# Kernel optimization log

Measured on AMD Instinct MI355X. Metric: run time of the kernel, lower is better.

Reference implementation:

```python
import jax, jax.numpy as jnp
import numpy as np

EPS_NORM = 1e-9   # l2_norm eps in original
EPS_ENT = 1e-15   # PyG dense_diff_pool entropy eps


def _sage_block(x, adj, Wl, bl, Wr):
    """SAGEConv(aggr='mean') + ReLU + row L2-norm.
    x: [b,N,din], adj: [b,N,N] binary (adj[i,j]=1 means edge i->j).
    PyG mean-aggr for target j = mean over sources i: (A^T x)/max(deg_in,1).
    out = lin_l(aggr) + lin_r(x); lin_l has bias, lin_r does not.
    """
    deg = jnp.sum(adj, axis=1)                                  # [b,N] in-degree of targets
    agg = jnp.einsum('bij,bid->bjd', adj, x) / jnp.maximum(deg, 1.0)[..., None]
    h = jnp.einsum('bnd,od->bno', agg, Wl) + bl + jnp.einsum('bnd,od->bno', x, Wr)
    h = jax.nn.relu(h)
    return h / (jnp.linalg.norm(h, axis=-1, keepdims=True) + EPS_NORM)


def setup_inputs() -> dict:
    key = jax.random.key(0)
    ks = jax.random.split(key, 16)
    b, N, din, dh, K = 8, 2048, 128, 128, 128
    x = jax.random.normal(ks[0], (b, N, din), dtype=jnp.float32)
    # binary adjacency, avg in-degree ~ 0.01*N ~ 20
    adj = (jax.random.uniform(ks[1], (b, N, N)) < 0.01).astype(jnp.float32)

    def lin(k, o, i):
        return (jax.random.normal(k, (o, i), dtype=jnp.float32) / np.sqrt(i)).astype(jnp.float32)

    return {
        'x': x, 'adj': adj,
        'We1l': lin(ks[2], dh, din), 'be1': jnp.zeros((dh,), jnp.float32), 'We1r': lin(ks[3], dh, din),
        'We2l': lin(ks[4], dh, dh),  'be2': jnp.zeros((dh,), jnp.float32), 'We2r': lin(ks[5], dh, dh),
        'Wa1l': lin(ks[6], dh, din), 'ba1': jnp.zeros((dh,), jnp.float32), 'Wa1r': lin(ks[7], dh, din),
        'Wa2l': lin(ks[8], K, dh),   'ba2': jnp.zeros((K,), jnp.float32), 'Wa2r': lin(ks[9], K, dh),
    }


def reference(x, adj, We1l, be1, We1r, We2l, be2, We2r, Wa1l, ba1, Wa1r, Wa2l, ba2, Wa2r):
    # embedding GNN
    h = _sage_block(x, adj, We1l, be1, We1r)
    h_emb = _sage_block(h, adj, We2l, be2, We2r)          # [b,N,dh]
    # assignment GNN
    a = _sage_block(x, adj, Wa1l, ba1, Wa1r)
    a = _sage_block(a, adj, Wa2l, ba2, Wa2r)              # [b,N,K]
    S = jax.nn.softmax(a, axis=-1)                        # [b,N,K]
    # dense_diff_pool
    h_pooled = jnp.einsum('bnk,bnd->bkd', S, h_emb)       # [b,K,dh]
    adj_pooled = jnp.einsum('bnk,bnm,bml->bkl', S, adj, S)  # [b,K,K]
    link = adj - jnp.einsum('bnk,bmk->bnm', S, S)
    link_loss = jnp.linalg.norm(link) / adj.size          # global Frobenius / numel
    ent_loss = jnp.mean(jnp.sum(-S * jnp.log(S + EPS_ENT), axis=-1))
    return h_pooled, adj_pooled, link_loss, ent_loss
```

## Files before the change

### kernel.cpp

```cpp
#include <hip/hip_runtime.h>
#include <hip/hip_bf16.h>
#include <math.h>

#define BB 8
#define NN 2048
#define DD 128
#define SPL 16
#define CAPQ 32

typedef __bf16 bf16x8 __attribute__((ext_vector_type(8)));
typedef float f32x4 __attribute__((ext_vector_type(4)));

__device__ inline unsigned short f2bu(float f) {
  __hip_bfloat16 h = __float2bfloat16(f);
  return *reinterpret_cast<unsigned short*>(&h);
}
__device__ inline unsigned int pack2(float a, float b) {
  return (unsigned int)f2bu(a) | ((unsigned int)f2bu(b) << 16);
}
__device__ inline float blo(unsigned u) { return __uint_as_float(u << 16); }
__device__ inline float bhi(unsigned u) { return __uint_as_float(u & 0xffff0000u); }

__global__ __launch_bounds__(256) void k_build(const float* __restrict__ adj,
                                               unsigned short* __restrict__ colidx,
                                               float* __restrict__ deg,
                                               float* __restrict__ rdeg,
                                               double* __restrict__ scal) {
  __shared__ float T[2][64][65];
  __shared__ unsigned short L[64][4][CAPQ];
  __shared__ int cnts[64][4];
  __shared__ float tsum[64];
  int b = blockIdx.y, j0 = blockIdx.x * 64;
  const float* A = adj + (size_t)b * NN * NN + j0;
  int t = threadIdx.x;
  int lr = t >> 2, lc0 = (t & 3) * 16;
  int sc = t & 63, sq = t >> 6;
  float4 pre[4];
  #pragma unroll
  for (int e = 0; e < 4; ++e)
    pre[e] = *(const float4*)(A + (size_t)lr * NN + lc0 + e * 4);
  #pragma unroll
  for (int e = 0; e < 4; ++e)
    *(float4*)&T[0][lr][lc0 + e * 4] = pre[e];
  __syncthreads();
  int cnt = 0;
  for (int ch = 0; ch < 32; ++ch) {
    if (ch + 1 < 32) {
      const float* src = A + (size_t)(ch + 1) * 64 * NN;
      #pragma unroll
      for (int e = 0; e < 4; ++e)
        pre[e] = *(const float4*)(src + (size_t)lr * NN + lc0 + e * 4);
    }
    #pragma unroll
    for (int p = 0; p < 16; ++p) {
      int il = sq * 16 + p;
      float v = T[ch & 1][il][sc];
      if (v != 0.f) {
        L[sc][sq][cnt < CAPQ ? cnt : CAPQ - 1] = (unsigned short)(ch * 64 + il);
        ++cnt;
      }
    }
    if (ch + 1 < 32) {
      #pragma unroll
      for (int e = 0; e < 4; ++e)
        *(float4*)&T[(ch + 1) & 1][lr][lc0 + e * 4] = pre[e];
    }
    __syncthreads();
  }
  cnts[sc][sq] = cnt;
  __syncthreads();
  int c = t >> 2, seg = t & 3;
  int n0 = cnts[c][0], n1 = cnts[c][1], n2 = cnts[c][2], n3 = cnts[c][3];
  int tot = n0 + n1 + n2 + n3;
  unsigned short vals[16];
  #pragma unroll
  for (int e = 0; e < 16; ++e) {
    int k = seg * 16 + e;
    unsigned short x = 0;
    if (k < n0) x = L[c][0][k];
    else if (k < n0 + n1) x = L[c][1][k - n0];
    else if (k < n0 + n1 + n2) x = L[c][2][k - n0 - n1];
    else if (k < tot) x = L[c][3][k - n0 - n1 - n2];
    vals[e] = x;
  }
  unsigned short* dst = colidx + ((size_t)b * NN + j0 + c) * 64 + seg * 16;
  *(uint4*)dst = *(uint4*)&vals[0];
  *(uint4*)(dst + 8) = *(uint4*)&vals[8];
  if (seg == 0) {
    size_t gj = (size_t)b * NN + j0 + c;
    deg[gj] = (float)tot;
    rdeg[gj] = 1.f / fmaxf((float)tot, 1.f);
    tsum[c] = (float)tot;
  }
  __syncthreads();
  if (t < 64) {
    float s = tsum[t];
    #pragma unroll
    for (int off = 32; off > 0; off >>= 1) s += __shfl_xor(s, off);
    if (t == 0) atomicAdd(scal, (double)s);
  }
}

__global__ __launch_bounds__(256) void k_xbf(const float* __restrict__ x,
                                             __hip_bfloat16* __restrict__ xb) {
  size_t i8 = ((size_t)blockIdx.x * 256 + threadIdx.x) * 8;
  float4 a = *(const float4*)(x + i8);
  float4 b2 = *(const float4*)(x + i8 + 4);
  unsigned r[4] = {pack2(a.x, a.y), pack2(a.z, a.w), pack2(b2.x, b2.y), pack2(b2.z, b2.w)};
  *(uint4*)((unsigned short*)xb + i8) = *(uint4*)r;
}

__global__ __launch_bounds__(256) void k_agg(const __hip_bfloat16* __restrict__ V,
                                             const unsigned short* __restrict__ colidx,
                                             const float* __restrict__ deg,
                                             const float* __restrict__ rdeg,
                                             __hip_bfloat16* __restrict__ out) {
  int w = threadIdx.x >> 6, l = threadIdx.x & 63;
  size_t jg = (size_t)blockIdx.x * 4 + w;
  int b = (int)(jg >> 11);
  int cnt = (int)deg[jg];
  int myi = colidx[jg * 64 + l];
  const unsigned short* Vb = (const unsigned short*)V + (((size_t)b << 11)) * DD;
  float ax = 0.f, ay = 0.f;
  int k = 0;
  for (; k + 4 <= cnt; k += 4) {
    int i0 = __shfl(myi, k), i1 = __shfl(myi, k + 1);
    int i2 = __shfl(myi, k + 2), i3 = __shfl(myi, k + 3);
    unsigned u0 = *(const unsigned*)(Vb + (size_t)i0 * DD + 2 * l);
    unsigned u1 = *(const unsigned*)(Vb + (size_t)i1 * DD + 2 * l);
    unsigned u2 = *(const unsigned*)(Vb + (size_t)i2 * DD + 2 * l);
    unsigned u3 = *(const unsigned*)(Vb + (size_t)i3 * DD + 2 * l);
    ax += blo(u0) + blo(u1) + blo(u2) + blo(u3);
    ay += bhi(u0) + bhi(u1) + bhi(u2) + bhi(u3);
  }
  for (; k < cnt; ++k) {
    int i0 = __shfl(myi, k);
    unsigned u0 = *(const unsigned*)(Vb + (size_t)i0 * DD + 2 * l);
    ax += blo(u0); ay += bhi(u0);
  }
  float sc = rdeg[jg];
  *(unsigned*)((unsigned short*)out + jg * DD + 2 * l) = pack2(ax * sc, ay * sc);
}

__global__ __launch_bounds__(256) void k_agg2(const __hip_bfloat16* __restrict__ V1,
                                              const __hip_bfloat16* __restrict__ V2,
                                              const unsigned short* __restrict__ colidx,
                                              const float* __restrict__ deg,
                                              const float* __restrict__ rdeg,
                                              __hip_bfloat16* __restrict__ out1,
                                              __hip_bfloat16* __restrict__ out2) {
  int w = threadIdx.x >> 6, l = threadIdx.x & 63;
  size_t jg = (size_t)blockIdx.x * 4 + w;
  int b = (int)(jg >> 11);
  int cnt = (int)deg[jg];
  int myi = colidx[jg * 64 + l];
  size_t base = (((size_t)b << 11)) * DD + 2 * l;
  const unsigned short* Va = (const unsigned short*)V1 + base;
  const unsigned short* Vb = (const unsigned short*)V2 + base;
  float ax = 0.f, ay = 0.f, bx = 0.f, by = 0.f;
  int k = 0;
  for (; k + 2 <= cnt; k += 2) {
    int i0 = __shfl(myi, k), i1 = __shfl(myi, k + 1);
    unsigned a0 = *(const unsigned*)(Va + (size_t)i0 * DD);
    unsigned a1 = *(const unsigned*)(Va + (size_t)i1 * DD);
    unsigned b0 = *(const unsigned*)(Vb + (size_t)i0 * DD);
    unsigned b1 = *(const unsigned*)(Vb + (size_t)i1 * DD);
    ax += blo(a0) + blo(a1); ay += bhi(a0) + bhi(a1);
    bx += blo(b0) + blo(b1); by += bhi(b0) + bhi(b1);
  }
  if (k < cnt) {
    int i0 = __shfl(myi, k);
    unsigned a0 = *(const unsigned*)(Va + (size_t)i0 * DD);
    unsigned b0 = *(const unsigned*)(Vb + (size_t)i0 * DD);
    ax += blo(a0); ay += bhi(a0);
    bx += blo(b0); by += bhi(b0);
  }
  float sc = rdeg[jg];
  *(unsigned*)((unsigned short*)out1 + jg * DD + 2 * l) = pack2(ax * sc, ay * sc);
  *(unsigned*)((unsigned short*)out2 + jg * DD + 2 * l) = pack2(bx * sc, by * sc);
}

__global__ __launch_bounds__(256) void k_aggT(const __hip_bfloat16* __restrict__ Sbf,
                                              const unsigned short* __restrict__ colidx,
                                              const float* __restrict__ deg,
                                              __hip_bfloat16* __restrict__ PT) {
  __shared__ float Lt[128][17];
  int w = threadIdx.x >> 6, l = threadIdx.x & 63;
  size_t jbase = (size_t)blockIdx.x * 16;
  int b = (int)(jbase >> 11);
  const unsigned short* Vb = (const unsigned short*)Sbf + (((size_t)b << 11)) * DD;
  #pragma unroll
  for (int cc = 0; cc < 4; ++cc) {
    int jl = w * 4 + cc;
    size_t jg = jbase + jl;
    int cnt = (int)deg[jg];
    int myi = colidx[jg * 64 + l];
    float ax = 0.f, ay = 0.f;
    int k = 0;
    for (; k + 4 <= cnt; k += 4) {
      int i0 = __shfl(myi, k), i1 = __shfl(myi, k + 1);
      int i2 = __shfl(myi, k + 2), i3 = __shfl(myi, k + 3);
      unsigned u0 = *(const unsigned*)(Vb + (size_t)i0 * DD + 2 * l);
      unsigned u1 = *(const unsigned*)(Vb + (size_t)i1 * DD + 2 * l);
      unsigned u2 = *(const unsigned*)(Vb + (size_t)i2 * DD + 2 * l);
      unsigned u3 = *(const unsigned*)(Vb + (size_t)i3 * DD + 2 * l);
      ax += blo(u0) + blo(u1) + blo(u2) + blo(u3);
      ay += bhi(u0) + bhi(u1) + bhi(u2) + bhi(u3);
    }
    for (; k < cnt; ++k) {
      int i0 = __shfl(myi, k);
      unsigned u0 = *(const unsigned*)(Vb + (size_t)i0 * DD + 2 * l);
      ax += blo(u0); ay += bhi(u0);
    }
    Lt[2 * l][jl] = ax;
    Lt[2 * l + 1][jl] = ay;
  }
  __syncthreads();
  int t = threadIdx.x;
  if (t < 128) {
    int j0 = (int)(jbase & (NN - 1));
    unsigned wv[8];
    #pragma unroll
    for (int e = 0; e < 8; ++e)
      wv[e] = pack2(Lt[t][2 * e], Lt[t][2 * e + 1]);
    unsigned short* dst = (unsigned short*)PT + ((size_t)b * DD + t) * NN + j0;
    *(uint4*)dst = *(uint4*)&wv[0];
    *(uint4*)(dst + 8) = *(uint4*)&wv[4];
  }
}

__global__ __launch_bounds__(256) void k_linred(const __hip_bfloat16* __restrict__ AGG,
                                                const __hip_bfloat16* __restrict__ X2,
                                                const float* __restrict__ W1,
                                                const float* __restrict__ W2,
                                                const float* __restrict__ bias,
                                                float* __restrict__ outf,
                                                __hip_bfloat16* __restrict__ outbf,
                                                __hip_bfloat16* __restrict__ outT) {
  __shared__ __align__(16) char smem[64 * 136 * 2 * 2];
  __shared__ __align__(16) __hip_bfloat16 Wsm[128 * 72];
  __shared__ float bsm[128];
  __hip_bfloat16* As = (__hip_bfloat16*)smem;
  __hip_bfloat16* Xs = As + 64 * 136;
  float* Ho = (float*)smem;

  int b = blockIdx.y, j0 = blockIdx.x * 64;
  int t = threadIdx.x;
  size_t rowbase = (size_t)b * NN + j0;

  if (t < 128) bsm[t] = bias[t];
  #pragma unroll
  for (int e = 0; e < 8; ++e) {
    int idx = t + e * 256;
    int r = idx >> 5, c4 = idx & 31;
    size_t g = (rowbase + r) * DD + c4 * 4;
    *(uint2*)&As[r * 136 + c4 * 4] = *(const uint2*)((const unsigned short*)AGG + g);
    *(uint2*)&Xs[r * 136 + c4 * 4] = *(const uint2*)((const unsigned short*)X2 + g);
  }
  __syncthreads();

  int w = t >> 6, l = t & 63;
  int lm = l & 15, lq = l >> 4;
  int jloc = w * 16 + lm;
  f32x4 acc[8];
  #pragma unroll
  for (int mt = 0; mt < 8; ++mt)
    #pragma unroll
    for (int r = 0; r < 4; ++r) acc[mt][r] = 0.f;

  #pragma unroll
  for (int ph = 0; ph < 2; ++ph) {
    const __hip_bfloat16* Xt = ph ? Xs : As;
    const float* W = ph ? W2 : W1;
    #pragma unroll
    for (int ch = 0; ch < 2; ++ch) {
      __syncthreads();
      #pragma unroll
      for (int e = 0; e < 8; ++e) {
        int idx = t + e * 256;
        int o = idx >> 4, k4 = idx & 15;
        float4 wv = *(const float4*)(W + o * DD + ch * 64 + k4 * 4);
        uint2 pw; pw.x = pack2(wv.x, wv.y); pw.y = pack2(wv.z, wv.w);
        *(uint2*)&Wsm[o * 72 + k4 * 4] = pw;
      }
      __syncthreads();
      #pragma unroll
      for (int s = 0; s < 2; ++s) {
        int kx = ch * 64 + s * 32 + lq * 8;
        bf16x8 bfr = *(const bf16x8*)&Xt[jloc * 136 + kx];
        int kw = s * 32 + lq * 8;
        #pragma unroll
        for (int mt = 0; mt < 8; ++mt) {
          bf16x8 afr = *(const bf16x8*)&Wsm[(mt * 16 + lm) * 72 + kw];
          acc[mt] = __builtin_amdgcn_mfma_f32_16x16x32_bf16(afr, bfr, acc[mt], 0, 0, 0);
        }
      }
    }
  }

  __syncthreads();
  float hv[8][4];
  float psum = 0.f;
  #pragma unroll
  for (int mt = 0; mt < 8; ++mt)
    #pragma unroll
    for (int r = 0; r < 4; ++r) {
      int o = mt * 16 + lq * 4 + r;
      float v = fmaxf(acc[mt][r] + bsm[o], 0.f);
      hv[mt][r] = v;
      psum += v * v;
    }
  psum += __shfl_xor(psum, 16);
  psum += __shfl_xor(psum, 32);
  float rn = 1.f / (sqrtf(psum) + 1e-9f);
  #pragma unroll
  for (int mt = 0; mt < 8; ++mt)
    #pragma unroll
    for (int r = 0; r < 4; ++r) {
      int o = mt * 16 + lq * 4 + r;
      Ho[jloc * 132 + o] = hv[mt][r] * rn;
    }
  __syncthreads();
  if (outf) {
    #pragma unroll
    for (int e = 0; e < 8; ++e) {
      int idx = t + e * 256;
      int r = idx >> 5, c4 = idx & 31;
      float4 v = *(const float4*)&Ho[r * 132 + c4 * 4];
      *(float4*)(outf + (rowbase + r) * DD + c4 * 4) = v;
    }
  }
  if (outbf) {
    #pragma unroll
    for (int e = 0; e < 4; ++e) {
      int idx = t + e * 256;
      int r = idx >> 4, c8 = idx & 15;
      const float* h = &Ho[r * 132 + c8 * 8];
      unsigned pk[4] = {pack2(h[0], h[1]), pack2(h[2], h[3]),
                        pack2(h[4], h[5]), pack2(h[6], h[7])};
      *(uint4*)((unsigned short*)outbf + (rowbase + r) * DD + c8 * 8) = *(uint4*)pk;
    }
  }
  if (outT) {
    int d = t >> 1, half = t & 1;
    unsigned wv[16];
    #pragma unroll
    for (int e = 0; e < 16; ++e)
      wv[e] = pack2(Ho[(half * 32 + 2 * e) * 132 + d], Ho[(half * 32 + 2 * e + 1) * 132 + d]);
    unsigned short* dst = (unsigned short*)outT + ((size_t)b * DD + d) * NN + j0 + half * 32;
    #pragma unroll
    for (int q = 0; q < 4; ++q)
      *(uint4*)(dst + q * 8) = *(uint4*)&wv[q * 4];
  }
}

__global__ __launch_bounds__(256) void k_softmax64(const float* __restrict__ A2,
                                                   __hip_bfloat16* __restrict__ Sbf,
                                                   __hip_bfloat16* __restrict__ STt,
                                                   double* __restrict__ scal) {
  __shared__ float T[128][65];
  __shared__ float red[256];
  int b = blockIdx.y, j0 = blockIdx.x * 64;
  int t = threadIdx.x;
  int r = t >> 2, q = t & 3;
  const float* Ar = A2 + ((size_t)b * NN + j0 + r) * DD + q * 32;
  float v[32];
  #pragma unroll
  for (int e = 0; e < 8; ++e) *(float4*)&v[e * 4] = *(const float4*)&Ar[e * 4];
  float m = v[0];
  #pragma unroll
  for (int i = 1; i < 32; ++i) m = fmaxf(m, v[i]);
  m = fmaxf(m, __shfl_xor(m, 1));
  m = fmaxf(m, __shfl_xor(m, 2));
  float sum = 0.f;
  #pragma unroll
  for (int i = 0; i < 32; ++i) { v[i] = expf(v[i] - m); sum += v[i]; }
  sum += __shfl_xor(sum, 1);
  sum += __shfl_xor(sum, 2);
  float inv = 1.f / sum;
  float ent = 0.f;
  #pragma unroll
  for (int i = 0; i < 32; ++i) {
    float p = v[i] * inv;
    v[i] = p;
    ent -= p * logf(p + 1e-15f);
    T[q * 32 + i][r] = p;
  }
  unsigned pk[16];
  #pragma unroll
  for (int e = 0; e < 16; ++e) pk[e] = pack2(v[2 * e], v[2 * e + 1]);
  unsigned short* sd = (unsigned short*)Sbf + ((size_t)b * NN + j0 + r) * DD + q * 32;
  #pragma unroll
  for (int e = 0; e < 4; ++e)
    *(uint4*)(sd + e * 8) = *(uint4*)&pk[e * 4];
  red[t] = ent;
  __syncthreads();
  for (int off = 128; off > 0; off >>= 1) {
    if (t < off) red[t] += red[t + off];
    __syncthreads();
  }
  if (t == 0) atomicAdd(scal + 3, (double)red[0]);
  int d = t >> 1, half = t & 1;
  unsigned wv[16];
  #pragma unroll
  for (int e = 0; e < 16; ++e)
    wv[e] = pack2(T[d][half * 32 + 2 * e], T[d][half * 32 + 2 * e + 1]);
  unsigned short* dst = (unsigned short*)STt + ((size_t)b * DD + d) * NN + j0 + half * 32;
  #pragma unroll
  for (int p = 0; p < 4; ++p)
    *(uint4*)(dst + p * 8) = *(uint4*)&wv[p * 4];
}

__global__ __launch_bounds__(256) void k_tnm(const __hip_bfloat16* __restrict__ ST,
                                             const __hip_bfloat16* __restrict__ HT,
                                             const __hip_bfloat16* __restrict__ PT,
                                             float* __restrict__ part) {
  __shared__ __align__(16) __hip_bfloat16 As[128 * 64];
  __shared__ __align__(16) __hip_bfloat16 Bs[128 * 64];
  int pb = blockIdx.y;
  int pair = pb >> 3, b = pb & 7;
  const __hip_bfloat16* Xa = (pair == 1) ? PT : ST;
  const __hip_bfloat16* Ya = (pair == 0) ? HT : ST;
  const __hip_bfloat16* Ab = Xa + (size_t)b * DD * NN;
  const __hip_bfloat16* Bb = Ya + (size_t)b * DD * NN;
  int k0 = blockIdx.x * (NN / SPL);
  int tid = threadIdx.x;
  int w = tid >> 6, l = tid & 63;
  int wj = w & 1, wd = w >> 1;
  int sr = l >> 3, ss = l & 7;
  int lm = l & 15, lq = l >> 4;
  f32x4 acc[4][4];
  #pragma unroll
  for (int a = 0; a < 4; ++a)
    #pragma unroll
    for (int c = 0; c < 4; ++c)
      #pragma unroll
      for (int r = 0; r < 4; ++r) acc[a][c][r] = 0.f;

  for (int kb = 0; kb < (NN / SPL) / 64; ++kb) {
    int kbase = k0 + kb * 64;
    __syncthreads();
    #pragma unroll
    for (int e = 0; e < 4; ++e) {
      int r = 32 * w + 8 * e + sr;
      int g = ss ^ (r & 7);
      const __hip_bfloat16* srcA = Ab + (size_t)r * NN + kbase + g * 8;
      __builtin_amdgcn_global_load_lds(
          (const __attribute__((address_space(1))) void*)srcA,
          (__attribute__((address_space(3))) void*)&As[(32 * w + 8 * e) * 64], 16, 0, 0);
      const __hip_bfloat16* srcB = Bb + (size_t)r * NN + kbase + g * 8;
      __builtin_amdgcn_global_load_lds(
          (const __attribute__((address_space(1))) void*)srcB,
          (__attribute__((address_space(3))) void*)&Bs[(32 * w + 8 * e) * 64], 16, 0, 0);
    }
    __syncthreads();
    #pragma unroll
    for (int ks = 0; ks < 2; ++ks) {
      bf16x8 afr[4], bfr[4];
      int kg = ks * 4 + lq;
      #pragma unroll
      for (int jt = 0; jt < 4; ++jt) {
        int jl = wj * 64 + jt * 16 + lm;
        afr[jt] = *(const bf16x8*)&As[jl * 64 + ((kg ^ (jl & 7)) << 3)];
      }
      #pragma unroll
      for (int dt = 0; dt < 4; ++dt) {
        int dl = wd * 64 + dt * 16 + lm;
        bfr[dt] = *(const bf16x8*)&Bs[dl * 64 + ((kg ^ (dl & 7)) << 3)];
      }
      #pragma unroll
      for (int jt = 0; jt < 4; ++jt)
        #pragma unroll
        for (int dt = 0; dt < 4; ++dt)
          acc[jt][dt] = __builtin_amdgcn_mfma_f32_16x16x32_bf16(afr[jt], bfr[dt], acc[jt][dt], 0, 0, 0);
    }
  }
  float* P = part + ((size_t)(pair * SPL + blockIdx.x) * BB + b) * DD * DD;
  #pragma unroll
  for (int jt = 0; jt < 4; ++jt)
    #pragma unroll
    for (int reg = 0; reg < 4; ++reg) {
      int j = wj * 64 + jt * 16 + lq * 4 + reg;
      float* row = P + (size_t)j * DD;
      #pragma unroll
      for (int dt = 0; dt < 4; ++dt)
        row[wd * 64 + dt * 16 + lm] = acc[jt][dt][reg];
    }
}

__global__ __launch_bounds__(256) void k_tnred3(const float* __restrict__ part,
                                                float* __restrict__ out,
                                                double* __restrict__ scal) {
  __shared__ float red[256];
  int pair = blockIdx.y;
  size_t i = (size_t)blockIdx.x * 256 + threadIdx.x;
  float s = 0.f;
  #pragma unroll
  for (int ks = 0; ks < SPL; ++ks)
    s += part[((size_t)pair * SPL + ks) * (BB * DD * DD) + i];
  float contrib = 0.f;
  if (pair == 0) {
    out[i] = s;
  } else if (pair == 1) {
    out[(size_t)BB * DD * DD + i] = s;
    int rc = (int)(i & (DD * DD - 1));
    if ((rc >> 7) == (rc & 127)) contrib = s;
  } else {
    contrib = s * s;
  }
  red[threadIdx.x] = contrib;
  __syncthreads();
  for (int off = 128; off > 0; off >>= 1) {
    if (threadIdx.x < off) red[threadIdx.x] += red[threadIdx.x + off];
    __syncthreads();
  }
  if (threadIdx.x == 0 && pair != 0 && red[0] != 0.f)
    atomicAdd(scal + pair, (double)red[0]);
}

__global__ void k_final(const double* __restrict__ scal, float* __restrict__ out) {
  if (threadIdx.x == 0 && blockIdx.x == 0) {
    double link2 = scal[0] - 2.0 * scal[1] + scal[2];
    if (link2 < 0.0) link2 = 0.0;
    out[2 * BB * DD * DD]     = (float)(sqrt(link2) / (double)((size_t)BB * NN * NN));
    out[2 * BB * DD * DD + 1] = (float)(scal[3] / (double)(BB * NN));
  }
}

extern "C" void kernel_launch(void* const* d_in, const int* in_sizes, int n_in,
                              void* d_out, int out_size, void* d_ws, size_t ws_size,
                              hipStream_t stream) {
  const float* x    = (const float*)d_in[0];
  const float* adj  = (const float*)d_in[1];
  const float* We1l = (const float*)d_in[2];
  const float* be1  = (const float*)d_in[3];
  const float* We1r = (const float*)d_in[4];
  const float* We2l = (const float*)d_in[5];
  const float* be2  = (const float*)d_in[6];
  const float* We2r = (const float*)d_in[7];
  const float* Wa1l = (const float*)d_in[8];
  const float* ba1  = (const float*)d_in[9];
  const float* Wa1r = (const float*)d_in[10];
  const float* Wa2l = (const float*)d_in[11];
  const float* ba2  = (const float*)d_in[12];
  const float* Wa2r = (const float*)d_in[13];
  float* out = (float*)d_out;

  const size_t MB = 1 << 20;
  char* ws = (char*)d_ws;
  double* scal = (double*)ws;
  float* deg   = (float*)(ws + 256);
  float* rdeg  = (float*)(ws + 256 + 65536);
  unsigned short* colidx = (unsigned short*)(ws + 1 * MB);
  __hip_bfloat16* xbf   = (__hip_bfloat16*)(ws + 3 * MB);
  __hip_bfloat16* agg1  = (__hip_bfloat16*)(ws + 7 * MB);
  __hip_bfloat16* agg2h = (__hip_bfloat16*)(ws + 11 * MB);
  __hip_bfloat16* a1bf  = (__hip_bfloat16*)(ws + 15 * MB);
  __hip_bfloat16* h1bf  = (__hip_bfloat16*)(ws + 19 * MB);
  float* a2f            = (float*)(ws + 23 * MB);
  __hip_bfloat16* Sbf   = (__hip_bfloat16*)(ws + 31 * MB);
  __hip_bfloat16* STt   = (__hip_bfloat16*)(ws + 35 * MB);
  __hip_bfloat16* h2T   = (__hip_bfloat16*)(ws + 39 * MB);
  __hip_bfloat16* PT    = (__hip_bfloat16*)(ws + 43 * MB);
  float* part           = (float*)(ws + 47 * MB);

  hipMemsetAsync(scal, 0, 4 * sizeof(double), stream);

  dim3 gb(32, 8), glr(32, 8), gsm(32, 8), gtm(SPL, 24), gtr(512, 3);

  k_build<<<gb, 256, 0, stream>>>(adj, colidx, deg, rdeg, scal);
  k_xbf<<<1024, 256, 0, stream>>>(x, xbf);
  k_agg<<<4096, 256, 0, stream>>>(xbf, colidx, deg, rdeg, agg1);
  k_linred<<<glr, 256, 0, stream>>>(agg1, xbf, We1l, We1r, be1, nullptr, h1bf, nullptr);
  k_linred<<<glr, 256, 0, stream>>>(agg1, xbf, Wa1l, Wa1r, ba1, nullptr, a1bf, nullptr);
  k_agg2<<<4096, 256, 0, stream>>>(a1bf, h1bf, colidx, deg, rdeg, agg1, agg2h);
  k_linred<<<glr, 256, 0, stream>>>(agg1, a1bf, Wa2l, Wa2r, ba2, a2f, nullptr, nullptr);
  k_linred<<<glr, 256, 0, stream>>>(agg2h, h1bf, We2l, We2r, be2, nullptr, nullptr, h2T);
  k_softmax64<<<gsm, 256, 0, stream>>>(a2f, Sbf, STt, scal);
  k_aggT<<<1024, 256, 0, stream>>>(Sbf, colidx, deg, PT);
  k_tnm<<<gtm, 256, 0, stream>>>(STt, h2T, PT, part);
  k_tnred3<<<gtr, 256, 0, stream>>>(part, out, scal);
  k_final<<<1, 64, 0, stream>>>(scal, out);
}
```

Baseline: 362.0 us.

## Fuse launches: merge xbf into build, pair linear layers, drop atomics and memset

Folds the x-to-bf16 conversion into the adjacency build kernel and runs the two first-layer linear transforms in one kernel that shares the staged inputs. The two second-layer linear kernels become a single launch split on blockIdx.z. Double atomics, the memset and the final scalar accumulation are replaced by per-block partial sums reduced in k_final. This is meant to cut launch overhead and redundant input loads, at the cost of higher shared-memory and register use in k_lin2 and float rather than double partial sums.

```diff
diff --git a/kernel.cpp b/kernel.cpp
--- a/kernel.cpp
+++ b/kernel.cpp
@@ -22,15 +22,18 @@
 __device__ inline float bhi(unsigned u) { return __uint_as_float(u & 0xffff0000u); }
 
 __global__ __launch_bounds__(256) void k_build(const float* __restrict__ adj,
+                                               const float* __restrict__ x,
                                                unsigned short* __restrict__ colidx,
                                                float* __restrict__ deg,
                                                float* __restrict__ rdeg,
-                                               double* __restrict__ scal) {
+                                               float* __restrict__ nnzpart,
+                                               __hip_bfloat16* __restrict__ xb) {
   __shared__ float T[2][64][65];
   __shared__ unsigned short L[64][4][CAPQ];
   __shared__ int cnts[64][4];
   __shared__ float tsum[64];
   int b = blockIdx.y, j0 = blockIdx.x * 64;
+  int linear = blockIdx.y * 32 + blockIdx.x;
   const float* A = adj + (size_t)b * NN * NN + j0;
   int t = threadIdx.x;
   int lr = t >> 2, lc0 = (t & 3) * 16;
@@ -76,12 +79,12 @@
   #pragma unroll
   for (int e = 0; e < 16; ++e) {
     int k = seg * 16 + e;
-    unsigned short x = 0;
-    if (k < n0) x = L[c][0][k];
-    else if (k < n0 + n1) x = L[c][1][k - n0];
-    else if (k < n0 + n1 + n2) x = L[c][2][k - n0 - n1];
-    else if (k < tot) x = L[c][3][k - n0 - n1 - n2];
-    vals[e] = x;
+    unsigned short xv = 0;
+    if (k < n0) xv = L[c][0][k];
+    else if (k < n0 + n1) xv = L[c][1][k - n0];
+    else if (k < n0 + n1 + n2) xv = L[c][2][k - n0 - n1];
+    else if (k < tot) xv = L[c][3][k - n0 - n1 - n2];
+    vals[e] = xv;
   }
   unsigned short* dst = colidx + ((size_t)b * NN + j0 + c) * 64 + seg * 16;
   *(uint4*)dst = *(uint4*)&vals[0];
@@ -97,17 +100,16 @@
     float s = tsum[t];
     #pragma unroll
     for (int off = 32; off > 0; off >>= 1) s += __shfl_xor(s, off);
-    if (t == 0) atomicAdd(scal, (double)s);
-  }
-}
-
-__global__ __launch_bounds__(256) void k_xbf(const float* __restrict__ x,
-                                             __hip_bfloat16* __restrict__ xb) {
-  size_t i8 = ((size_t)blockIdx.x * 256 + threadIdx.x) * 8;
-  float4 a = *(const float4*)(x + i8);
-  float4 b2 = *(const float4*)(x + i8 + 4);
-  unsigned r[4] = {pack2(a.x, a.y), pack2(a.z, a.w), pack2(b2.x, b2.y), pack2(b2.z, b2.w)};
-  *(uint4*)((unsigned short*)xb + i8) = *(uint4*)r;
+    if (t == 0) nnzpart[linear] = s;
+  }
+  size_t base = (size_t)linear * 8192;
+  #pragma unroll
+  for (int e = 0; e < 8; ++e) {
+    size_t off = base + e * 1024 + t * 4;
+    float4 a = *(const float4*)(x + off);
+    unsigned r2[2] = {pack2(a.x, a.y), pack2(a.z, a.w)};
+    *(uint2*)((unsigned short*)xb + off) = *(uint2*)r2;
+  }
 }
 
 __global__ __launch_bounds__(256) void k_agg(const __hip_bfloat16* __restrict__ V,
@@ -229,14 +231,128 @@
   }
 }
 
-__global__ __launch_bounds__(256) void k_linred(const __hip_bfloat16* __restrict__ AGG,
-                                                const __hip_bfloat16* __restrict__ X2,
-                                                const float* __restrict__ W1,
-                                                const float* __restrict__ W2,
-                                                const float* __restrict__ bias,
-                                                float* __restrict__ outf,
-                                                __hip_bfloat16* __restrict__ outbf,
-                                                __hip_bfloat16* __restrict__ outT) {
+__global__ __launch_bounds__(256) void k_lin2(const __hip_bfloat16* __restrict__ AGG,
+                                              const __hip_bfloat16* __restrict__ X2,
+                                              const float* __restrict__ W0a,
+                                              const float* __restrict__ W0b,
+                                              const float* __restrict__ b0,
+                                              const float* __restrict__ W1a,
+                                              const float* __restrict__ W1b,
+                                              const float* __restrict__ b1,
+                                              __hip_bfloat16* __restrict__ out0,
+                                              __hip_bfloat16* __restrict__ out1) {
+  __shared__ __align__(16) char smem[64 * 136 * 2 * 2];
+  __shared__ __align__(16) __hip_bfloat16 Wsm[2][128 * 72];
+  __shared__ float bsm[2][128];
+  __hip_bfloat16* As = (__hip_bfloat16*)smem;
+  __hip_bfloat16* Xs = As + 64 * 136;
+  float* Ho = (float*)smem;
+
+  int b = blockIdx.y, j0 = blockIdx.x * 64;
+  int t = threadIdx.x;
+  size_t rowbase = (size_t)b * NN + j0;
+
+  if (t < 128) { bsm[0][t] = b0[t]; bsm[1][t] = b1[t]; }
+  #pragma unroll
+  for (int e = 0; e < 8; ++e) {
+    int idx = t + e * 256;
+    int r = idx >> 5, c4 = idx & 31;
+    size_t g = (rowbase + r) * DD + c4 * 4;
+    *(uint2*)&As[r * 136 + c4 * 4] = *(const uint2*)((const unsigned short*)AGG + g);
+    *(uint2*)&Xs[r * 136 + c4 * 4] = *(const uint2*)((const unsigned short*)X2 + g);
+  }
+  __syncthreads();
+
+  int w = t >> 6, l = t & 63;
+  int lm = l & 15, lq = l >> 4;
+  int jloc = w * 16 + lm;
+  f32x4 acc0[8], acc1[8];
+  #pragma unroll
+  for (int mt = 0; mt < 8; ++mt)
+    #pragma unroll
+    for (int r = 0; r < 4; ++r) { acc0[mt][r] = 0.f; acc1[mt][r] = 0.f; }
+
+  #pragma unroll
+  for (int ph = 0; ph < 2; ++ph) {
+    const __hip_bfloat16* Xt = ph ? Xs : As;
+    const float* Wx = ph ? W0b : W0a;
+    const float* Wy = ph ? W1b : W1a;
+    #pragma unroll
+    for (int ch = 0; ch < 2; ++ch) {
+      __syncthreads();
+      #pragma unroll
+      for (int e = 0; e < 8; ++e) {
+        int idx = t + e * 256;
+        int o = idx >> 4, k4 = idx & 15;
+        float4 wv = *(const float4*)(Wx + o * DD + ch * 64 + k4 * 4);
+        uint2 pw; pw.x = pack2(wv.x, wv.y); pw.y = pack2(wv.z, wv.w);
+        *(uint2*)&Wsm[0][o * 72 + k4 * 4] = pw;
+        float4 wv2 = *(const float4*)(Wy + o * DD + ch * 64 + k4 * 4);
+        uint2 pw2; pw2.x = pack2(wv2.x, wv2.y); pw2.y = pack2(wv2.z, wv2.w);
+        *(uint2*)&Wsm[1][o * 72 + k4 * 4] = pw2;
+      }
+      __syncthreads();
+      #pragma unroll
+      for (int s = 0; s < 2; ++s) {
+        int kx = ch * 64 + s * 32 + lq * 8;
+        bf16x8 bfr = *(const bf16x8*)&Xt[jloc * 136 + kx];
+        int kw = s * 32 + lq * 8;
+        #pragma unroll
+        for (int mt = 0; mt < 8; ++mt) {
+          bf16x8 a0 = *(const bf16x8*)&Wsm[0][(mt * 16 + lm) * 72 + kw];
+          acc0[mt] = __builtin_amdgcn_mfma_f32_16x16x32_bf16(a0, bfr, acc0[mt], 0, 0, 0);
+          bf16x8 a1 = *(const bf16x8*)&Wsm[1][(mt * 16 + lm) * 72 + kw];
+          acc1[mt] = __builtin_amdgcn_mfma_f32_16x16x32_bf16(a1, bfr, acc1[mt], 0, 0, 0);
+        }
+      }
+    }
+  }
+
+  #pragma unroll
+  for (int set = 0; set < 2; ++set) {
+    __syncthreads();
+    f32x4* acc = set ? acc1 : acc0;
+    float psum = 0.f;
+    float hv[8][4];
+    #pragma unroll
+    for (int mt = 0; mt < 8; ++mt)
+      #pragma unroll
+      for (int r = 0; r < 4; ++r) {
+        int o = mt * 16 + lq * 4 + r;
+        float v = fmaxf(acc[mt][r] + bsm[set][o], 0.f);
+        hv[mt][r] = v;
+        psum += v * v;
+      }
+    psum += __shfl_xor(psum, 16);
+    psum += __shfl_xor(psum, 32);
+    float rn = 1.f / (sqrtf(psum) + 1e-9f);
+    #pragma unroll
+    for (int mt = 0; mt < 8; ++mt)
+      #pragma unroll
+      for (int r = 0; r < 4; ++r) {
+        int o = mt * 16 + lq * 4 + r;
+        Ho[jloc * 132 + o] = hv[mt][r] * rn;
+      }
+    __syncthreads();
+    __hip_bfloat16* ob = set ? out1 : out0;
+    #pragma unroll
+    for (int e = 0; e < 4; ++e) {
+      int idx = t + e * 256;
+      int r = idx >> 4, c8 = idx & 15;
+      const float* h = &Ho[r * 132 + c8 * 8];
+      unsigned pk[4] = {pack2(h[0], h[1]), pack2(h[2], h[3]),
+                        pack2(h[4], h[5]), pack2(h[6], h[7])};
+      *(uint4*)((unsigned short*)ob + (rowbase + r) * DD + c8 * 8) = *(uint4*)pk;
+    }
+  }
+}
+
+__device__ __forceinline__ void linred_body(const __hip_bfloat16* AGG,
+                                            const __hip_bfloat16* X2,
+                                            const float* W1, const float* W2,
+                                            const float* bias,
+                                            float* outf, __hip_bfloat16* outT,
+                                            int bx, int by) {
   __shared__ __align__(16) char smem[64 * 136 * 2 * 2];
   __shared__ __align__(16) __hip_bfloat16 Wsm[128 * 72];
   __shared__ float bsm[128];
@@ -244,7 +360,7 @@
   __hip_bfloat16* Xs = As + 64 * 136;
   float* Ho = (float*)smem;
 
-  int b = blockIdx.y, j0 = blockIdx.x * 64;
+  int b = by, j0 = bx * 64;
   int t = threadIdx.x;
   size_t rowbase = (size_t)b * NN + j0;
 
@@ -330,17 +446,6 @@
       *(float4*)(outf + (rowbase + r) * DD + c4 * 4) = v;
     }
   }
-  if (outbf) {
-    #pragma unroll
-    for (int e = 0; e < 4; ++e) {
-      int idx = t + e * 256;
-      int r = idx >> 4, c8 = idx & 15;
-      const float* h = &Ho[r * 132 + c8 * 8];
-      unsigned pk[4] = {pack2(h[0], h[1]), pack2(h[2], h[3]),
-                        pack2(h[4], h[5]), pack2(h[6], h[7])};
-      *(uint4*)((unsigned short*)outbf + (rowbase + r) * DD + c8 * 8) = *(uint4*)pk;
-    }
-  }
   if (outT) {
     int d = t >> 1, half = t & 1;
     unsigned wv[16];
@@ -354,10 +459,28 @@
   }
 }
 
+__global__ __launch_bounds__(256) void k_linz(const __hip_bfloat16* __restrict__ AG0,
+                                              const __hip_bfloat16* __restrict__ X0,
+                                              const float* __restrict__ W0a,
+                                              const float* __restrict__ W0b,
+                                              const float* __restrict__ b0,
+                                              float* __restrict__ out0f,
+                                              const __hip_bfloat16* __restrict__ AG1,
+                                              const __hip_bfloat16* __restrict__ X1,
+                                              const float* __restrict__ W1a,
+                                              const float* __restrict__ W1b,
+                                              const float* __restrict__ b1,
+                                              __hip_bfloat16* __restrict__ out1T) {
+  if (blockIdx.z == 0)
+    linred_body(AG0, X0, W0a, W0b, b0, out0f, nullptr, blockIdx.x, blockIdx.y);
+  else
+    linred_body(AG1, X1, W1a, W1b, b1, nullptr, out1T, blockIdx.x, blockIdx.y);
+}
+
 __global__ __launch_bounds__(256) void k_softmax64(const float* __restrict__ A2,
                                                    __hip_bfloat16* __restrict__ Sbf,
                                                    __hip_bfloat16* __restrict__ STt,
-                                                   double* __restrict__ scal) {
+                                                   float* __restrict__ entpart) {
   __shared__ float T[128][65];
   __shared__ float red[256];
   int b = blockIdx.y, j0 = blockIdx.x * 64;
@@ -399,7 +522,7 @@
     if (t < off) red[t] += red[t + off];
     __syncthreads();
   }
-  if (t == 0) atomicAdd(scal + 3, (double)red[0]);
+  if (t == 0) entpart[blockIdx.y * 32 + blockIdx.x] = red[0];
   int d = t >> 1, half = t & 1;
   unsigned wv[16];
   #pragma unroll
@@ -490,7 +613,8 @@
 
 __global__ __launch_bounds__(256) void k_tnred3(const float* __restrict__ part,
                                                 float* __restrict__ out,
-                                                double* __restrict__ scal) {
+                                                float* __restrict__ trpart,
+                                                float* __restrict__ sqpart) {
   __shared__ float red[256];
   int pair = blockIdx.y;
   size_t i = (size_t)blockIdx.x * 256 + threadIdx.x;
@@ -514,16 +638,38 @@
     if (threadIdx.x < off) red[threadIdx.x] += red[threadIdx.x + off];
     __syncthreads();
   }
-  if (threadIdx.x == 0 && pair != 0 && red[0] != 0.f)
-    atomicAdd(scal + pair, (double)red[0]);
-}
-
-__global__ void k_final(const double* __restrict__ scal, float* __restrict__ out) {
-  if (threadIdx.x == 0 && blockIdx.x == 0) {
-    double link2 = scal[0] - 2.0 * scal[1] + scal[2];
+  if (threadIdx.x == 0) {
+    if (pair == 1) trpart[blockIdx.x] = red[0];
+    else if (pair == 2) sqpart[blockIdx.x] = red[0];
+  }
+}
+
+__global__ __launch_bounds__(256) void k_final(const float* __restrict__ nnzpart,
+                                               const float* __restrict__ entpart,
+                                               const float* __restrict__ trpart,
+                                               const float* __restrict__ sqpart,
+                                               float* __restrict__ out) {
+  __shared__ float4 red[256];
+  int t = threadIdx.x;
+  float4 v;
+  v.x = nnzpart[t];
+  v.y = entpart[t];
+  v.z = trpart[t] + trpart[t + 256];
+  v.w = sqpart[t] + sqpart[t + 256];
+  red[t] = v;
+  __syncthreads();
+  for (int off = 128; off > 0; off >>= 1) {
+    if (t < off) {
+      red[t].x += red[t + off].x; red[t].y += red[t + off].y;
+      red[t].z += red[t + off].z; red[t].w += red[t + off].w;
+    }
+    __syncthreads();
+  }
+  if (t == 0) {
+    double link2 = (double)red[0].x - 2.0 * (double)red[0].z + (double)red[0].w;
     if (link2 < 0.0) link2 = 0.0;
     out[2 * BB * DD * DD]     = (float)(sqrt(link2) / (double)((size_t)BB * NN * NN));
-    out[2 * BB * DD * DD + 1] = (float)(scal[3] / (double)(BB * NN));
+    out[2 * BB * DD * DD + 1] = (float)((double)red[0].y / (double)(BB * NN));
   }
 }
 
@@ -548,9 +694,12 @@
 
   const size_t MB = 1 << 20;
   char* ws = (char*)d_ws;
-  double* scal = (double*)ws;
-  float* deg   = (float*)(ws + 256);
-  float* rdeg  = (float*)(ws + 256 + 65536);
+  float* nnzpart = (float*)(ws);
+  float* entpart = (float*)(ws + 1024);
+  float* trpart  = (float*)(ws + 2048);
+  float* sqpart  = (float*)(ws + 4096);
+  float* deg     = (float*)(ws + 8192);
+  float* rdeg    = (float*)(ws + 8192 + 65536);
   unsigned short* colidx = (unsigned short*)(ws + 1 * MB);
   __hip_bfloat16* xbf   = (__hip_bfloat16*)(ws + 3 * MB);
   __hip_bfloat16* agg1  = (__hip_bfloat16*)(ws + 7 * MB);
@@ -564,21 +713,17 @@
   __hip_bfloat16* PT    = (__hip_bfloat16*)(ws + 43 * MB);
   float* part           = (float*)(ws + 47 * MB);
 
-  hipMemsetAsync(scal, 0, 4 * sizeof(double), stream);
-
-  dim3 gb(32, 8), glr(32, 8), gsm(32, 8), gtm(SPL, 24), gtr(512, 3);
-
-  k_build<<<gb, 256, 0, stream>>>(adj, colidx, deg, rdeg, scal);
-  k_xbf<<<1024, 256, 0, stream>>>(x, xbf);
+  dim3 gb(32, 8), glr(32, 8), glz(32, 8, 2), gsm(32, 8), gtm(SPL, 24), gtr(512, 3);
+
+  k_build<<<gb, 256, 0, stream>>>(adj, x, colidx, deg, rdeg, nnzpart, xbf);
   k_agg<<<4096, 256, 0, stream>>>(xbf, colidx, deg, rdeg, agg1);
-  k_linred<<<glr, 256, 0, stream>>>(agg1, xbf, We1l, We1r, be1, nullptr, h1bf, nullptr);
-  k_linred<<<glr, 256, 0, stream>>>(agg1, xbf, Wa1l, Wa1r, ba1, nullptr, a1bf, nullptr);
+  k_lin2<<<glr, 256, 0, stream>>>(agg1, xbf, We1l, We1r, be1, Wa1l, Wa1r, ba1, h1bf, a1bf);
   k_agg2<<<4096, 256, 0, stream>>>(a1bf, h1bf, colidx, deg, rdeg, agg1, agg2h);
-  k_linred<<<glr, 256, 0, stream>>>(agg1, a1bf, Wa2l, Wa2r, ba2, a2f, nullptr, nullptr);
-  k_linred<<<glr, 256, 0, stream>>>(agg2h, h1bf, We2l, We2r, be2, nullptr, nullptr, h2T);
-  k_softmax64<<<gsm, 256, 0, stream>>>(a2f, Sbf, STt, scal);
+  k_linz<<<glz, 256, 0, stream>>>(agg1, a1bf, Wa2l, Wa2r, ba2, a2f,
+                                  agg2h, h1bf, We2l, We2r, be2, h2T);
+  k_softmax64<<<gsm, 256, 0, stream>>>(a2f, Sbf, STt, entpart);
   k_aggT<<<1024, 256, 0, stream>>>(Sbf, colidx, deg, PT);
   k_tnm<<<gtm, 256, 0, stream>>>(STt, h2T, PT, part);
-  k_tnred3<<<gtr, 256, 0, stream>>>(part, out, scal);
-  k_final<<<1, 64, 0, stream>>>(scal, out);
-}
+  k_tnred3<<<gtr, 256, 0, stream>>>(part, out, trpart, sqpart);
+  k_final<<<1, 256, 0, stream>>>(nnzpart, entpart, trpart, sqpart, out);
+}
```

New measurement: 336.9 us. -6.9%, faster.
